# Performance work log

Hardware: AMD Instinct MI355X
Metric: run time of the kernel (lower is better)

Reference implementation:

```python
import jax, jax.numpy as jnp
import numpy as np

N = 40000      # nodes
E = 640000     # edges
G = 2048       # graphs
D = 128        # emb_dim
T = 10         # num_tasks
L = 5          # layers
ATOM_VOCAB = 64
BOND_VOCAB = 8
BN_EPS = 1e-5


def _bn(x, g, b, m, v):
    # inference-mode BatchNorm1d with running stats
    return (x - m) * jax.lax.rsqrt(v + BN_EPS) * g + b


def setup_inputs() -> dict:
    key = jax.random.key(0)
    ks = jax.random.split(key, 24)
    inp = {
        "x_atom": jax.random.randint(ks[0], (N, 9), 0, ATOM_VOCAB),
        "edge_index": jax.random.randint(ks[1], (2, E), 0, N),
        "edge_attr": jax.random.randint(ks[2], (E, 3), 0, BOND_VOCAB),
        "batch": jnp.sort(jax.random.randint(ks[3], (N,), 0, G)),
        # embedding tables
        "atom_emb": jax.random.normal(ks[4], (9, ATOM_VOCAB, D)) * 0.1,
        "bond_emb": jax.random.normal(ks[5], (L, 3, BOND_VOCAB, D)) * 0.1,
        # per-layer GIN params (stacked over L)
        "eps": jnp.zeros((L,)),
        "W1": jax.random.normal(ks[6], (L, D, 2 * D)) * 0.05,
        "b1": jnp.zeros((L, 2 * D)),
        "g1": jnp.ones((L, 2 * D)),
        "bt1": jnp.zeros((L, 2 * D)),
        "m1": jax.random.normal(ks[7], (L, 2 * D)) * 0.1,
        "v1": jax.random.uniform(ks[8], (L, 2 * D), minval=0.5, maxval=1.5),
        "W2": jax.random.normal(ks[9], (L, 2 * D, D)) * 0.05,
        "b2": jnp.zeros((L, D)),
        # outer BatchNorm per layer
        "gO": jnp.ones((L, D)),
        "btO": jnp.zeros((L, D)),
        "mO": jax.random.normal(ks[10], (L, D)) * 0.1,
        "vO": jax.random.uniform(ks[11], (L, D), minval=0.5, maxval=1.5),
        # prediction head
        "Wp": jax.random.normal(ks[12], (D, T)) * 0.05,
        "bp": jnp.zeros((T,)),
    }
    return inp


def reference(x_atom, edge_index, edge_attr, batch, atom_emb, bond_emb, eps,
              W1, b1, g1, bt1, m1, v1, W2, b2, gO, btO, mO, vO, Wp, bp):
    src, dst = edge_index[0], edge_index[1]
    # AtomEncoder: sum of per-feature embeddings -> [N, D]
    x = atom_emb[jnp.arange(9)[None, :], x_atom].sum(axis=1)
    feat3 = jnp.arange(3)[None, :]
    for i in range(L):
        # BondEncoder for this layer -> [E, D]
        e = bond_emb[i][feat3, edge_attr].sum(axis=1)
        # message: relu(x_j + edge_emb); aggregate: scatter-add at dst
        msg = jax.nn.relu(x[src] + e)
        agg = jax.ops.segment_sum(msg, dst, num_segments=N)
        h = (1.0 + eps[i]) * x + agg
        # MLP: Linear -> BN -> ReLU -> Linear
        h = jax.nn.relu(_bn(h @ W1[i] + b1[i], g1[i], bt1[i], m1[i], v1[i]))
        h = h @ W2[i] + b2[i]
        # outer BN; ReLU after all but last layer (dropout = identity in eval)
        x = _bn(h, gO[i], btO[i], mO[i], vO[i])
        if i < L - 1:
            x = jax.nn.relu(x)
    # global mean pool over graphs
    sums = jax.ops.segment_sum(x, batch, num_segments=G)
    cnt = jax.ops.segment_sum(jnp.ones((N,), x.dtype), batch, num_segments=G)
    pooled = sums / jnp.maximum(cnt, 1.0)[:, None]
    return pooled @ Wp + bp
```

## Files before the change

### kernel.cpp

```cpp
#include <hip/hip_runtime.h>
#include <hip/hip_bf16.h>

#define NN 40000
#define NE 640000
#define NG 2048
#define DD 128
#define NT 10
#define NL 5
#define NB 80

typedef __attribute__((ext_vector_type(8))) short short8;
typedef __attribute__((ext_vector_type(4))) float f32x4;
typedef unsigned short ushort_t;

static __device__ __forceinline__ ushort_t f2b(float f) {
    return __bfloat16_as_ushort(__float2bfloat16(f));
}
static __device__ __forceinline__ float b2f(ushort_t u) {
    return __bfloat162float(__ushort_as_bfloat16(u));
}

__global__ void __launch_bounds__(256)
k_setup(const float* __restrict__ W1, const float* __restrict__ W2,
        const float* __restrict__ bemb, const int* __restrict__ xa,
        const float* __restrict__ aemb, const int* __restrict__ ei,
        ushort_t* __restrict__ W1P, ushort_t* __restrict__ W2P,
        ushort_t* __restrict__ ebsum16, ushort_t* __restrict__ x16,
        int* __restrict__ deg) {
    int b = blockIdx.x, t = threadIdx.x;
    if (b < 1280) {
        int tid = b * 256 + t;
        int layer = tid >> 16;
        int r = tid & 65535;
        int half = r >> 15;
        int q = r & 32767;
        int j = q & 7;
        int lane = (q >> 3) & 63;
        if (half == 0) {
            int kk = (q >> 9) & 3;
            int nt = q >> 11;
            int n = nt * 16 + (lane & 15);
            int k = kk * 32 + (lane >> 4) * 8 + j;
            W1P[layer * 32768 + q] = f2b(W1[(layer * DD + k) * 256 + n]);
        } else {
            int kk = (q >> 9) & 7;
            int nt = q >> 12;
            int n = nt * 16 + (lane & 15);
            int k = kk * 32 + (lane >> 4) * 8 + j;
            W2P[layer * 32768 + q] = f2b(W2[(layer * 256 + k) * DD + n]);
        }
        int d = tid & 127;
        int c = (tid >> 7) & 511;
        const float* bl = bemb + (size_t)layer * 3 * 8 * DD;
        ebsum16[tid] = f2b(bl[(c & 7) * DD + d] + bl[(8 + ((c >> 3) & 7)) * DD + d] +
                           bl[(16 + (c >> 6)) * DD + d]);
    } else if (b < 21280) {
        int half = t >> 7, d = t & 127;
        int n = (b - 1280) * 2 + half;
        __shared__ int idx[2][9];
        if (d < 9) idx[half][d] = xa[n * 9 + d];
        __syncthreads();
        float s = 0.f;
#pragma unroll
        for (int f = 0; f < 9; ++f) s += aemb[(f * 64 + idx[half][f]) * DD + d];
        x16[n * DD + d] = f2b(s);
    } else {
        int e = (b - 21280) * 256 + t;
        atomicAdd(&deg[ei[NE + e]], 1);
    }
}


__global__ void k_scan1(const int* __restrict__ deg, int* __restrict__ off,
                        int* __restrict__ blksum) {
    int b = blockIdx.x, t = threadIdx.x;
    int i = b * 256 + t;
    __shared__ int s[256];
    int v = (i < NN) ? deg[i] : 0;
    s[t] = v;
    __syncthreads();
    for (int d = 1; d < 256; d <<= 1) {
        int add = (t >= d) ? s[t - d] : 0;
        __syncthreads();
        s[t] += add;
        __syncthreads();
    }
    if (i <= NN) off[i] = s[t] - v;
    if (t == 255) blksum[b] = s[255];
}

__global__ void k_scan2(int* __restrict__ blk) {
    int t = threadIdx.x;
    __shared__ int s[256];
    int v = blk[t];
    s[t] = v;
    __syncthreads();
    for (int d = 1; d < 256; d <<= 1) {
        int add = (t >= d) ? s[t - d] : 0;
        __syncthreads();
        s[t] += add;
        __syncthreads();
    }
    blk[256 + t] = s[t] - v;
}

__global__ void k_scan3(int* __restrict__ off, const int* __restrict__ blk) {
    int b = blockIdx.x, t = threadIdx.x;
    int i = b * 256 + t;
    if (i <= NN) off[i] += blk[256 + b];
}

__global__ void __launch_bounds__(256)
k_bucket(const int* __restrict__ ei, const int* __restrict__ ea,
         const int* __restrict__ off, int* __restrict__ gbk,
         int2* __restrict__ ebuf) {
    __shared__ int hist[NB];
    __shared__ int sbase[NB];
    int t = threadIdx.x;
    int e0 = blockIdx.x * 1024;
    if (t < NB) hist[t] = 0;
    __syncthreads();
    int rank[4], buck[4], rec[4], dstv[4];
#pragma unroll
    for (int k = 0; k < 4; ++k) {
        int e = e0 + k * 256 + t;
        int src = ei[e];
        int dst = ei[NE + e];
        int a0 = ea[e * 3 + 0], a1 = ea[e * 3 + 1], a2 = ea[e * 3 + 2];
        rec[k] = src | ((a0 | (a1 << 3) | (a2 << 6)) << 16);
        dstv[k] = dst;
        int b = dst >> 9;
        buck[k] = b;
        rank[k] = atomicAdd(&hist[b], 1);
    }
    __syncthreads();
    if (t < NB) sbase[t] = atomicAdd(&gbk[t], hist[t]);
    __syncthreads();
#pragma unroll
    for (int k = 0; k < 4; ++k) {
        int b = buck[k];
        int slot = off[b << 9] + sbase[b] + rank[k];
        ebuf[slot] = make_int2(rec[k], dstv[k]);
    }
}

__global__ void k_scatter2(const int2* __restrict__ ebuf, const int* __restrict__ off,
                           int* __restrict__ cursor, int2* __restrict__ epack) {
    int i = blockIdx.x * 256 + threadIdx.x;
    int2 s = ebuf[i];
    int dst = s.y;
    int p = off[dst] + atomicAdd(&cursor[dst], 1);
    epack[p] = make_int2(s.x & 0xFFFF, s.x >> 16);
}

__global__ void __launch_bounds__(256)
k_gather(const ushort_t* __restrict__ xin, const int* __restrict__ off,
         const int2* __restrict__ epack, const ushort_t* __restrict__ ebsum16,
         const float* __restrict__ eps, int layer, ushort_t* __restrict__ h16) {
    int t = threadIdx.x;
    int lane = t & 63;
    int n = blockIdx.x * 4 + (t >> 6);
    const ushort2* x2 = (const ushort2*)xin;
    const ushort2* eb2 = (const ushort2*)ebsum16;
    ushort2 xv = x2[n * 64 + lane];
    float es = 1.f + eps[layer];
    float ax = es * b2f(xv.x), ay = es * b2f(xv.y);
    int p = off[n], p1 = off[n + 1];

    int2 e[8], f[8];
    bool have = (p + 8 <= p1);
    if (have) {
#pragma unroll
        for (int k = 0; k < 8; ++k) e[k] = epack[p + k];
    }
    while (have) {
        int np = p + 8;
        bool nh = (np + 8 <= p1);
        if (nh) {
#pragma unroll
            for (int k = 0; k < 8; ++k) f[k] = epack[np + k];
        }
        ushort2 vv[8], ss[8];
#pragma unroll
        for (int k = 0; k < 8; ++k) {
            vv[k] = eb2[e[k].y * 64 + lane];
            ss[k] = x2[e[k].x * 64 + lane];
        }
#pragma unroll
        for (int k = 0; k < 8; ++k) {
            ax += fmaxf(b2f(vv[k].x) + b2f(ss[k].x), 0.f);
            ay += fmaxf(b2f(vv[k].y) + b2f(ss[k].y), 0.f);
        }
        p = np;
#pragma unroll
        for (int k = 0; k < 8; ++k) e[k] = f[k];
        have = nh;
    }
    if (p + 4 <= p1) {
        int2 e4[4];
#pragma unroll
        for (int k = 0; k < 4; ++k) e4[k] = epack[p + k];
        ushort2 vv[4], ss[4];
#pragma unroll
        for (int k = 0; k < 4; ++k) {
            vv[k] = eb2[e4[k].y * 64 + lane];
            ss[k] = x2[e4[k].x * 64 + lane];
        }
#pragma unroll
        for (int k = 0; k < 4; ++k) {
            ax += fmaxf(b2f(vv[k].x) + b2f(ss[k].x), 0.f);
            ay += fmaxf(b2f(vv[k].y) + b2f(ss[k].y), 0.f);
        }
        p += 4;
    }
    for (; p < p1; ++p) {
        int2 er = epack[p];
        ushort2 ev = eb2[er.y * 64 + lane];
        ushort2 sv = x2[er.x * 64 + lane];
        ax += fmaxf(b2f(ev.x) + b2f(sv.x), 0.f);
        ay += fmaxf(b2f(ev.y) + b2f(sv.y), 0.f);
    }
    ushort2 o;
    o.x = f2b(ax);
    o.y = f2b(ay);
    ((ushort2*)h16)[n * 64 + lane] = o;
}

__global__ void __launch_bounds__(256)
k_mlp_mfma(const ushort_t* __restrict__ h16, const ushort_t* __restrict__ W1P,
           const ushort_t* __restrict__ W2P, const float* __restrict__ b1,
           const float* __restrict__ g1, const float* __restrict__ bt1,
           const float* __restrict__ m1, const float* __restrict__ v1,
           const float* __restrict__ b2_, const float* __restrict__ gO,
           const float* __restrict__ btO, const float* __restrict__ mO,
           const float* __restrict__ vO, int relu, ushort_t* __restrict__ xout) {
    __shared__ ushort_t aS[32 * 136];
    __shared__ ushort_t mid[32 * 264];
    int t = threadIdx.x;
    int wave = t >> 6, lane = t & 63;
    int row0 = blockIdx.x * 32;
    int lrow = lane & 15, quad = lane >> 4;

#pragma unroll
    for (int ps = 0; ps < 2; ++ps) {
        int idx = ps * 256 + t;
        int r = idx >> 4, c = (idx & 15) * 8;
        *(short8*)&aS[r * 136 + c] = *(const short8*)&h16[(row0 + r) * DD + c];
    }
    __syncthreads();

    f32x4 acc1[2][4];
#pragma unroll
    for (int rt = 0; rt < 2; ++rt)
#pragma unroll
        for (int i = 0; i < 4; ++i) acc1[rt][i] = (f32x4){0.f, 0.f, 0.f, 0.f};
#pragma unroll
    for (int kk = 0; kk < 4; ++kk) {
        short8 af0 = *(const short8*)&aS[lrow * 136 + kk * 32 + quad * 8];
        short8 af1 = *(const short8*)&aS[(16 + lrow) * 136 + kk * 32 + quad * 8];
#pragma unroll
        for (int i = 0; i < 4; ++i) {
            int nt = wave * 4 + i;
            short8 bf = *(const short8*)&W1P[((nt * 4 + kk) * 64 + lane) * 8];
            acc1[0][i] = __builtin_amdgcn_mfma_f32_16x16x32_bf16(af0, bf, acc1[0][i], 0, 0, 0);
            acc1[1][i] = __builtin_amdgcn_mfma_f32_16x16x32_bf16(af1, bf, acc1[1][i], 0, 0, 0);
        }
    }
#pragma unroll
    for (int i = 0; i < 4; ++i) {
        int col = (wave * 4 + i) * 16 + lrow;
        float s1 = g1[col] * rsqrtf(v1[col] + 1e-5f);
        float sh = bt1[col] - (m1[col] - b1[col]) * s1;
#pragma unroll
        for (int rt = 0; rt < 2; ++rt)
#pragma unroll
            for (int r = 0; r < 4; ++r) {
                int row = rt * 16 + quad * 4 + r;
                float o = acc1[rt][i][r] * s1 + sh;
                mid[row * 264 + col] = f2b(fmaxf(o, 0.f));
            }
    }
    __syncthreads();

    f32x4 acc2[2][2];
#pragma unroll
    for (int rt = 0; rt < 2; ++rt)
#pragma unroll
        for (int i = 0; i < 2; ++i) acc2[rt][i] = (f32x4){0.f, 0.f, 0.f, 0.f};
#pragma unroll
    for (int kk = 0; kk < 8; ++kk) {
        short8 af0 = *(const short8*)&mid[lrow * 264 + kk * 32 + quad * 8];
        short8 af1 = *(const short8*)&mid[(16 + lrow) * 264 + kk * 32 + quad * 8];
#pragma unroll
        for (int i = 0; i < 2; ++i) {
            int nt = wave * 2 + i;
            short8 bf = *(const short8*)&W2P[((nt * 8 + kk) * 64 + lane) * 8];
            acc2[0][i] = __builtin_amdgcn_mfma_f32_16x16x32_bf16(af0, bf, acc2[0][i], 0, 0, 0);
            acc2[1][i] = __builtin_amdgcn_mfma_f32_16x16x32_bf16(af1, bf, acc2[1][i], 0, 0, 0);
        }
    }
#pragma unroll
    for (int i = 0; i < 2; ++i) {
        int col = (wave * 2 + i) * 16 + lrow;
        float s = gO[col] * rsqrtf(vO[col] + 1e-5f);
        float sh = btO[col] - (mO[col] - b2_[col]) * s;
#pragma unroll
        for (int rt = 0; rt < 2; ++rt)
#pragma unroll
            for (int r = 0; r < 4; ++r) {
                int row = rt * 16 + quad * 4 + r;
                float o = acc2[rt][i][r] * s + sh;
                if (relu) o = fmaxf(o, 0.f);
                xout[(row0 + row) * DD + col] = f2b(o);
            }
    }
}

__global__ void k_poolhead(const ushort_t* __restrict__ x16,
                           const int* __restrict__ batch,
                           const float* __restrict__ Wp, const float* __restrict__ bp,
                           float* __restrict__ out) {
    int g = blockIdx.x, d = threadIdx.x;
    int lo = 0, hi = NN;
    while (lo < hi) { int m = (lo + hi) >> 1; if (batch[m] < g) lo = m + 1; else hi = m; }
    int start = lo;
    hi = NN;
    while (lo < hi) { int m = (lo + hi) >> 1; if (batch[m] < g + 1) lo = m + 1; else hi = m; }
    int end = lo;
    float s = 0.f;
    for (int n = start; n < end; ++n) s += b2f(x16[n * DD + d]);
    float c = fmaxf((float)(end - start), 1.f);
    __shared__ float p[DD];
    p[d] = s / c;
    __syncthreads();
    if (d < NT) {
        float acc = bp[d];
#pragma unroll 8
        for (int k = 0; k < DD; ++k) acc = fmaf(p[k], Wp[k * NT + d], acc);
        out[g * NT + d] = acc;
    }
}

extern "C" void kernel_launch(void* const* d_in, const int* in_sizes, int n_in,
                              void* d_out, int out_size, void* d_ws, size_t ws_size,
                              hipStream_t stream) {
    const int* x_atom = (const int*)d_in[0];
    const int* edge_index = (const int*)d_in[1];
    const int* edge_attr = (const int*)d_in[2];
    const int* batch = (const int*)d_in[3];
    const float* atom_emb = (const float*)d_in[4];
    const float* bond_emb = (const float*)d_in[5];
    const float* eps = (const float*)d_in[6];
    const float* W1 = (const float*)d_in[7];
    const float* b1 = (const float*)d_in[8];
    const float* g1 = (const float*)d_in[9];
    const float* bt1 = (const float*)d_in[10];
    const float* m1 = (const float*)d_in[11];
    const float* v1 = (const float*)d_in[12];
    const float* W2 = (const float*)d_in[13];
    const float* b2 = (const float*)d_in[14];
    const float* gO = (const float*)d_in[15];
    const float* btO = (const float*)d_in[16];
    const float* mO = (const float*)d_in[17];
    const float* vO = (const float*)d_in[18];
    const float* Wp = (const float*)d_in[19];
    const float* bp = (const float*)d_in[20];

    ushort_t* x16a = (ushort_t*)d_ws;
    ushort_t* x16b = x16a + NN * DD;
    ushort_t* h16 = x16b + NN * DD;
    ushort_t* W1P = h16 + NN * DD;
    ushort_t* W2P = W1P + NL * 32768;
    ushort_t* ebsum16 = W2P + NL * 32768;
    int* deg = (int*)(ebsum16 + NL * 65536);
    int* off = deg + NN;
    int* blk = off + 40064;
    int* cursor = blk + 512;
    int* gbk = cursor + NN;
    int2* epack = (int2*)(gbk + 128);
    int2* ebuf = epack + NE;

    hipMemsetAsync(deg, 0, (NN + 40064 + 512 + NN + 128) * sizeof(int), stream);

    k_setup<<<23780, 256, 0, stream>>>(W1, W2, bond_emb, x_atom, atom_emb,
                                       edge_index, W1P, W2P, ebsum16, x16a, deg);
    k_scan1<<<157, 256, 0, stream>>>(deg, off, blk);
    k_scan2<<<1, 256, 0, stream>>>(blk);
    k_scan3<<<157, 256, 0, stream>>>(off, blk);
    k_bucket<<<NE / 1024, 256, 0, stream>>>(edge_index, edge_attr, off, gbk, ebuf);
    k_scatter2<<<NE / 256, 256, 0, stream>>>(ebuf, off, cursor, epack);

    for (int i = 0; i < NL; ++i) {
        ushort_t* xin = (i & 1) ? x16b : x16a;
        ushort_t* xout = (i & 1) ? x16a : x16b;
        k_gather<<<NN / 4, 256, 0, stream>>>(xin, off, epack, ebsum16 + i * 65536,
                                             eps, i, h16);
        k_mlp_mfma<<<NN / 32, 256, 0, stream>>>(
            h16, W1P + (size_t)i * 32768, W2P + (size_t)i * 32768, b1 + i * 256,
            g1 + i * 256, bt1 + i * 256, m1 + i * 256, v1 + i * 256, b2 + i * DD,
            gO + i * DD, btO + i * DD, mO + i * DD, vO + i * DD,
            (i < NL - 1) ? 1 : 0, xout);
    }
    k_poolhead<<<NG, DD, 0, stream>>>(x16b, batch, Wp, bp, (float*)d_out);
}
```

Measured before the change: 411.7 us.

## Gather edge messages with 16-byte loads, four edges per wave in parallel

```diff
diff --git a/kernel.cpp b/kernel.cpp
--- a/kernel.cpp
+++ b/kernel.cpp
@@ -153,77 +153,78 @@
     epack[p] = make_int2(s.x & 0xFFFF, s.x >> 16);
 }
 
-__global__ void __launch_bounds__(256)
+__global__ void __launch_bounds__(256, 8)
 k_gather(const ushort_t* __restrict__ xin, const int* __restrict__ off,
          const int2* __restrict__ epack, const ushort_t* __restrict__ ebsum16,
          const float* __restrict__ eps, int layer, ushort_t* __restrict__ h16) {
     int t = threadIdx.x;
     int lane = t & 63;
     int n = blockIdx.x * 4 + (t >> 6);
-    const ushort2* x2 = (const ushort2*)xin;
-    const ushort2* eb2 = (const ushort2*)ebsum16;
-    ushort2 xv = x2[n * 64 + lane];
-    float es = 1.f + eps[layer];
-    float ax = es * b2f(xv.x), ay = es * b2f(xv.y);
-    int p = off[n], p1 = off[n + 1];
-
-    int2 e[8], f[8];
-    bool have = (p + 8 <= p1);
-    if (have) {
-#pragma unroll
-        for (int k = 0; k < 8; ++k) e[k] = epack[p + k];
-    }
-    while (have) {
-        int np = p + 8;
-        bool nh = (np + 8 <= p1);
-        if (nh) {
-#pragma unroll
-            for (int k = 0; k < 8; ++k) f[k] = epack[np + k];
+    int g = lane >> 4;
+    int dcol = lane & 15;
+    const short8* x8 = (const short8*)xin;
+    const short8* eb8 = (const short8*)ebsum16;
+    int p0 = off[n], p1 = off[n + 1];
+
+    float acc[8];
+#pragma unroll
+    for (int k = 0; k < 8; ++k) acc[k] = 0.f;
+
+    short8 sR0{}, vR0{}, sR1{}, vR1{};
+    bool mR0 = false, mR1 = false;
+    int2 eI{};
+    bool mI = false;
+
+    if (p0 < p1) {
+        bool m = (p0 + g < p1);
+        int2 e = epack[m ? (p0 + g) : p0];
+        if (m) { sR0 = x8[(size_t)e.x * 16 + dcol]; vR0 = eb8[e.y * 16 + dcol]; }
+        mR0 = m;
+    }
+    if (p0 + 4 < p1) {
+        bool m = (p0 + 4 + g < p1);
+        int2 e = epack[m ? (p0 + 4 + g) : (p0 + 4)];
+        if (m) { sR1 = x8[(size_t)e.x * 16 + dcol]; vR1 = eb8[e.y * 16 + dcol]; }
+        mR1 = m;
+    }
+    if (p0 + 8 < p1) {
+        mI = (p0 + 8 + g < p1);
+        eI = epack[mI ? (p0 + 8 + g) : (p0 + 8)];
+    }
+
+    for (int p = p0; p < p1; p += 4) {
+        short8 sR2{}, vR2{};
+        bool mR2 = mI;
+        if (mR2) { sR2 = x8[(size_t)eI.x * 16 + dcol]; vR2 = eb8[eI.y * 16 + dcol]; }
+        mI = false;
+        if (p + 12 < p1) {
+            mI = (p + 12 + g < p1);
+            eI = epack[mI ? (p + 12 + g) : (p + 12)];
         }
-        ushort2 vv[8], ss[8];
-#pragma unroll
-        for (int k = 0; k < 8; ++k) {
-            vv[k] = eb2[e[k].y * 64 + lane];
-            ss[k] = x2[e[k].x * 64 + lane];
+        if (mR0) {
+#pragma unroll
+            for (int k = 0; k < 8; ++k)
+                acc[k] += fmaxf(b2f((ushort_t)sR0[k]) + b2f((ushort_t)vR0[k]), 0.f);
         }
-#pragma unroll
-        for (int k = 0; k < 8; ++k) {
-            ax += fmaxf(b2f(vv[k].x) + b2f(ss[k].x), 0.f);
-            ay += fmaxf(b2f(vv[k].y) + b2f(ss[k].y), 0.f);
-        }
-        p = np;
-#pragma unroll
-        for (int k = 0; k < 8; ++k) e[k] = f[k];
-        have = nh;
-    }
-    if (p + 4 <= p1) {
-        int2 e4[4];
-#pragma unroll
-        for (int k = 0; k < 4; ++k) e4[k] = epack[p + k];
-        ushort2 vv[4], ss[4];
-#pragma unroll
-        for (int k = 0; k < 4; ++k) {
-            vv[k] = eb2[e4[k].y * 64 + lane];
-            ss[k] = x2[e4[k].x * 64 + lane];
-        }
-#pragma unroll
-        for (int k = 0; k < 4; ++k) {
-            ax += fmaxf(b2f(vv[k].x) + b2f(ss[k].x), 0.f);
-            ay += fmaxf(b2f(vv[k].y) + b2f(ss[k].y), 0.f);
-        }
-        p += 4;
-    }
-    for (; p < p1; ++p) {
-        int2 er = epack[p];
-        ushort2 ev = eb2[er.y * 64 + lane];
-        ushort2 sv = x2[er.x * 64 + lane];
-        ax += fmaxf(b2f(ev.x) + b2f(sv.x), 0.f);
-        ay += fmaxf(b2f(ev.y) + b2f(sv.y), 0.f);
-    }
-    ushort2 o;
-    o.x = f2b(ax);
-    o.y = f2b(ay);
-    ((ushort2*)h16)[n * 64 + lane] = o;
+        sR0 = sR1; vR0 = vR1; mR0 = mR1;
+        sR1 = sR2; vR1 = vR2; mR1 = mR2;
+    }
+
+#pragma unroll
+    for (int k = 0; k < 8; ++k) {
+        acc[k] += __shfl_xor(acc[k], 16, 64);
+        acc[k] += __shfl_xor(acc[k], 32, 64);
+    }
+
+    if (g == 0) {
+        float es = 1.f + eps[layer];
+        short8 xv = x8[(size_t)n * 16 + dcol];
+        short8 o;
+#pragma unroll
+        for (int k = 0; k < 8; ++k)
+            o[k] = (short)f2b(acc[k] + es * b2f((ushort_t)xv[k]));
+        *(short8*)&h16[(size_t)n * DD + dcol * 8] = o;
+    }
 }
 
 __global__ void __launch_bounds__(256)
```

Result: slower. 420.3 us (+2.1%).

## Pack edge records into one int and double MLP row tile to 64

Applied to the files above, without the earlier changes.

```diff
diff --git a/kernel.cpp b/kernel.cpp
--- a/kernel.cpp
+++ b/kernel.cpp
@@ -145,17 +145,17 @@
 }
 
 __global__ void k_scatter2(const int2* __restrict__ ebuf, const int* __restrict__ off,
-                           int* __restrict__ cursor, int2* __restrict__ epack) {
+                           int* __restrict__ cursor, int* __restrict__ epack) {
     int i = blockIdx.x * 256 + threadIdx.x;
     int2 s = ebuf[i];
     int dst = s.y;
     int p = off[dst] + atomicAdd(&cursor[dst], 1);
-    epack[p] = make_int2(s.x & 0xFFFF, s.x >> 16);
-}
-
-__global__ void __launch_bounds__(256)
+    epack[p] = s.x;
+}
+
+__global__ void __launch_bounds__(256, 8)
 k_gather(const ushort_t* __restrict__ xin, const int* __restrict__ off,
-         const int2* __restrict__ epack, const ushort_t* __restrict__ ebsum16,
+         const int* __restrict__ epack, const ushort_t* __restrict__ ebsum16,
          const float* __restrict__ eps, int layer, ushort_t* __restrict__ h16) {
     int t = threadIdx.x;
     int lane = t & 63;
@@ -167,7 +167,7 @@
     float ax = es * b2f(xv.x), ay = es * b2f(xv.y);
     int p = off[n], p1 = off[n + 1];
 
-    int2 e[8], f[8];
+    int e[8], f[8];
     bool have = (p + 8 <= p1);
     if (have) {
 #pragma unroll
@@ -183,8 +183,8 @@
         ushort2 vv[8], ss[8];
 #pragma unroll
         for (int k = 0; k < 8; ++k) {
-            vv[k] = eb2[e[k].y * 64 + lane];
-            ss[k] = x2[e[k].x * 64 + lane];
+            vv[k] = eb2[(e[k] >> 16) * 64 + lane];
+            ss[k] = x2[(e[k] & 0xFFFF) * 64 + lane];
         }
 #pragma unroll
         for (int k = 0; k < 8; ++k) {
@@ -197,14 +197,14 @@
         have = nh;
     }
     if (p + 4 <= p1) {
-        int2 e4[4];
+        int e4[4];
 #pragma unroll
         for (int k = 0; k < 4; ++k) e4[k] = epack[p + k];
         ushort2 vv[4], ss[4];
 #pragma unroll
         for (int k = 0; k < 4; ++k) {
-            vv[k] = eb2[e4[k].y * 64 + lane];
-            ss[k] = x2[e4[k].x * 64 + lane];
+            vv[k] = eb2[(e4[k] >> 16) * 64 + lane];
+            ss[k] = x2[(e4[k] & 0xFFFF) * 64 + lane];
         }
 #pragma unroll
         for (int k = 0; k < 4; ++k) {
@@ -214,9 +214,9 @@
         p += 4;
     }
     for (; p < p1; ++p) {
-        int2 er = epack[p];
-        ushort2 ev = eb2[er.y * 64 + lane];
-        ushort2 sv = x2[er.x * 64 + lane];
+        int er = epack[p];
+        ushort2 ev = eb2[(er >> 16) * 64 + lane];
+        ushort2 sv = x2[(er & 0xFFFF) * 64 + lane];
         ax += fmaxf(b2f(ev.x) + b2f(sv.x), 0.f);
         ay += fmaxf(b2f(ev.y) + b2f(sv.y), 0.f);
     }
@@ -234,36 +234,39 @@
            const float* __restrict__ b2_, const float* __restrict__ gO,
            const float* __restrict__ btO, const float* __restrict__ mO,
            const float* __restrict__ vO, int relu, ushort_t* __restrict__ xout) {
-    __shared__ ushort_t aS[32 * 136];
-    __shared__ ushort_t mid[32 * 264];
+    __shared__ ushort_t aS[64 * 136];
+    __shared__ ushort_t mid[64 * 264];
     int t = threadIdx.x;
     int wave = t >> 6, lane = t & 63;
-    int row0 = blockIdx.x * 32;
+    int row0 = blockIdx.x * 64;
     int lrow = lane & 15, quad = lane >> 4;
 
 #pragma unroll
-    for (int ps = 0; ps < 2; ++ps) {
+    for (int ps = 0; ps < 4; ++ps) {
         int idx = ps * 256 + t;
         int r = idx >> 4, c = (idx & 15) * 8;
         *(short8*)&aS[r * 136 + c] = *(const short8*)&h16[(row0 + r) * DD + c];
     }
     __syncthreads();
 
-    f32x4 acc1[2][4];
-#pragma unroll
-    for (int rt = 0; rt < 2; ++rt)
+    f32x4 acc1[4][4];
+#pragma unroll
+    for (int rt = 0; rt < 4; ++rt)
 #pragma unroll
         for (int i = 0; i < 4; ++i) acc1[rt][i] = (f32x4){0.f, 0.f, 0.f, 0.f};
 #pragma unroll
     for (int kk = 0; kk < 4; ++kk) {
-        short8 af0 = *(const short8*)&aS[lrow * 136 + kk * 32 + quad * 8];
-        short8 af1 = *(const short8*)&aS[(16 + lrow) * 136 + kk * 32 + quad * 8];
+        short8 af[4];
+#pragma unroll
+        for (int rt = 0; rt < 4; ++rt)
+            af[rt] = *(const short8*)&aS[(rt * 16 + lrow) * 136 + kk * 32 + quad * 8];
 #pragma unroll
         for (int i = 0; i < 4; ++i) {
             int nt = wave * 4 + i;
             short8 bf = *(const short8*)&W1P[((nt * 4 + kk) * 64 + lane) * 8];
-            acc1[0][i] = __builtin_amdgcn_mfma_f32_16x16x32_bf16(af0, bf, acc1[0][i], 0, 0, 0);
-            acc1[1][i] = __builtin_amdgcn_mfma_f32_16x16x32_bf16(af1, bf, acc1[1][i], 0, 0, 0);
+#pragma unroll
+            for (int rt = 0; rt < 4; ++rt)
+                acc1[rt][i] = __builtin_amdgcn_mfma_f32_16x16x32_bf16(af[rt], bf, acc1[rt][i], 0, 0, 0);
         }
     }
 #pragma unroll
@@ -272,7 +275,7 @@
         float s1 = g1[col] * rsqrtf(v1[col] + 1e-5f);
         float sh = bt1[col] - (m1[col] - b1[col]) * s1;
 #pragma unroll
-        for (int rt = 0; rt < 2; ++rt)
+        for (int rt = 0; rt < 4; ++rt)
 #pragma unroll
             for (int r = 0; r < 4; ++r) {
                 int row = rt * 16 + quad * 4 + r;
@@ -282,21 +285,24 @@
     }
     __syncthreads();
 
-    f32x4 acc2[2][2];
-#pragma unroll
-    for (int rt = 0; rt < 2; ++rt)
+    f32x4 acc2[4][2];
+#pragma unroll
+    for (int rt = 0; rt < 4; ++rt)
 #pragma unroll
         for (int i = 0; i < 2; ++i) acc2[rt][i] = (f32x4){0.f, 0.f, 0.f, 0.f};
 #pragma unroll
     for (int kk = 0; kk < 8; ++kk) {
-        short8 af0 = *(const short8*)&mid[lrow * 264 + kk * 32 + quad * 8];
-        short8 af1 = *(const short8*)&mid[(16 + lrow) * 264 + kk * 32 + quad * 8];
+        short8 af[4];
+#pragma unroll
+        for (int rt = 0; rt < 4; ++rt)
+            af[rt] = *(const short8*)&mid[(rt * 16 + lrow) * 264 + kk * 32 + quad * 8];
 #pragma unroll
         for (int i = 0; i < 2; ++i) {
             int nt = wave * 2 + i;
             short8 bf = *(const short8*)&W2P[((nt * 8 + kk) * 64 + lane) * 8];
-            acc2[0][i] = __builtin_amdgcn_mfma_f32_16x16x32_bf16(af0, bf, acc2[0][i], 0, 0, 0);
-            acc2[1][i] = __builtin_amdgcn_mfma_f32_16x16x32_bf16(af1, bf, acc2[1][i], 0, 0, 0);
+#pragma unroll
+            for (int rt = 0; rt < 4; ++rt)
+                acc2[rt][i] = __builtin_amdgcn_mfma_f32_16x16x32_bf16(af[rt], bf, acc2[rt][i], 0, 0, 0);
         }
     }
 #pragma unroll
@@ -305,7 +311,7 @@
         float s = gO[col] * rsqrtf(vO[col] + 1e-5f);
         float sh = btO[col] - (mO[col] - b2_[col]) * s;
 #pragma unroll
-        for (int rt = 0; rt < 2; ++rt)
+        for (int rt = 0; rt < 4; ++rt)
 #pragma unroll
             for (int r = 0; r < 4; ++r) {
                 int row = rt * 16 + quad * 4 + r;
@@ -377,8 +383,8 @@
     int* blk = off + 40064;
     int* cursor = blk + 512;
     int* gbk = cursor + NN;
-    int2* epack = (int2*)(gbk + 128);
-    int2* ebuf = epack + NE;
+    int* epack = gbk + 128;
+    int2* ebuf = (int2*)(epack + NE);
 
     hipMemsetAsync(deg, 0, (NN + 40064 + 512 + NN + 128) * sizeof(int), stream);
 
@@ -395,7 +401,7 @@
         ushort_t* xout = (i & 1) ? x16a : x16b;
         k_gather<<<NN / 4, 256, 0, stream>>>(xin, off, epack, ebsum16 + i * 65536,
                                              eps, i, h16);
-        k_mlp_mfma<<<NN / 32, 256, 0, stream>>>(
+        k_mlp_mfma<<<NN / 64, 256, 0, stream>>>(
             h16, W1P + (size_t)i * 32768, W2P + (size_t)i * 32768, b1 + i * 256,
             g1 + i * 256, bt1 + i * 256, m1 + i * 256, v1 + i * 256, b2 + i * DD,
             gO + i * DD, btO + i * DD, mO + i * DD, vO + i * DD,
```

Result: slower. 421.4 us (+2.4%).

## Gather neighbor features from an fp8 copy and pack edge records into one int

Applied to the files above, without the earlier changes.

```diff
diff --git a/kernel.cpp b/kernel.cpp
--- a/kernel.cpp
+++ b/kernel.cpp
@@ -12,12 +12,16 @@
 typedef __attribute__((ext_vector_type(8))) short short8;
 typedef __attribute__((ext_vector_type(4))) float f32x4;
 typedef unsigned short ushort_t;
+typedef unsigned char uchar_t;
 
 static __device__ __forceinline__ ushort_t f2b(float f) {
     return __bfloat16_as_ushort(__float2bfloat16(f));
 }
 static __device__ __forceinline__ float b2f(ushort_t u) {
     return __bfloat162float(__ushort_as_bfloat16(u));
+}
+static __device__ __forceinline__ uchar_t f2p8(float f) {
+    return (uchar_t)(__builtin_amdgcn_cvt_pk_fp8_f32(f, 0.f, 0, false) & 0xFF);
 }
 
 __global__ void __launch_bounds__(256)
@@ -26,7 +30,7 @@
         const float* __restrict__ aemb, const int* __restrict__ ei,
         ushort_t* __restrict__ W1P, ushort_t* __restrict__ W2P,
         ushort_t* __restrict__ ebsum16, ushort_t* __restrict__ x16,
-        int* __restrict__ deg) {
+        uchar_t* __restrict__ x8, int* __restrict__ deg) {
     int b = blockIdx.x, t = threadIdx.x;
     if (b < 1280) {
         int tid = b * 256 + t;
@@ -64,6 +68,7 @@
 #pragma unroll
         for (int f = 0; f < 9; ++f) s += aemb[(f * 64 + idx[half][f]) * DD + d];
         x16[n * DD + d] = f2b(s);
+        x8[n * DD + d] = f2p8(s);
     } else {
         int e = (b - 21280) * 256 + t;
         atomicAdd(&deg[ei[NE + e]], 1);
@@ -145,29 +150,31 @@
 }
 
 __global__ void k_scatter2(const int2* __restrict__ ebuf, const int* __restrict__ off,
-                           int* __restrict__ cursor, int2* __restrict__ epack) {
+                           int* __restrict__ cursor, int* __restrict__ epack) {
     int i = blockIdx.x * 256 + threadIdx.x;
     int2 s = ebuf[i];
     int dst = s.y;
     int p = off[dst] + atomicAdd(&cursor[dst], 1);
-    epack[p] = make_int2(s.x & 0xFFFF, s.x >> 16);
+    epack[p] = s.x;
 }
 
 __global__ void __launch_bounds__(256)
-k_gather(const ushort_t* __restrict__ xin, const int* __restrict__ off,
-         const int2* __restrict__ epack, const ushort_t* __restrict__ ebsum16,
-         const float* __restrict__ eps, int layer, ushort_t* __restrict__ h16) {
+k_gather(const ushort_t* __restrict__ xin, const uchar_t* __restrict__ x8in,
+         const int* __restrict__ off, const int* __restrict__ epack,
+         const ushort_t* __restrict__ ebsum16, const float* __restrict__ eps,
+         int layer, ushort_t* __restrict__ h16) {
     int t = threadIdx.x;
     int lane = t & 63;
     int n = blockIdx.x * 4 + (t >> 6);
     const ushort2* x2 = (const ushort2*)xin;
+    const ushort_t* x8r = (const ushort_t*)x8in;
     const ushort2* eb2 = (const ushort2*)ebsum16;
     ushort2 xv = x2[n * 64 + lane];
     float es = 1.f + eps[layer];
     float ax = es * b2f(xv.x), ay = es * b2f(xv.y);
     int p = off[n], p1 = off[n + 1];
 
-    int2 e[8], f[8];
+    int e[8], f[8];
     bool have = (p + 8 <= p1);
     if (have) {
 #pragma unroll
@@ -180,16 +187,19 @@
 #pragma unroll
             for (int k = 0; k < 8; ++k) f[k] = epack[np + k];
         }
-        ushort2 vv[8], ss[8];
+        ushort2 vv[8];
+        ushort_t sp[8];
 #pragma unroll
         for (int k = 0; k < 8; ++k) {
-            vv[k] = eb2[e[k].y * 64 + lane];
-            ss[k] = x2[e[k].x * 64 + lane];
+            vv[k] = eb2[(e[k] >> 16) * 64 + lane];
+            sp[k] = x8r[(e[k] & 0xFFFF) * 64 + lane];
         }
 #pragma unroll
         for (int k = 0; k < 8; ++k) {
-            ax += fmaxf(b2f(vv[k].x) + b2f(ss[k].x), 0.f);
-            ay += fmaxf(b2f(vv[k].y) + b2f(ss[k].y), 0.f);
+            float sx = __builtin_amdgcn_cvt_f32_fp8((int)sp[k], 0);
+            float sy = __builtin_amdgcn_cvt_f32_fp8((int)sp[k], 1);
+            ax += fmaxf(b2f(vv[k].x) + sx, 0.f);
+            ay += fmaxf(b2f(vv[k].y) + sy, 0.f);
         }
         p = np;
 #pragma unroll
@@ -197,28 +207,31 @@
         have = nh;
     }
     if (p + 4 <= p1) {
-        int2 e4[4];
+        int e4[4];
 #pragma unroll
         for (int k = 0; k < 4; ++k) e4[k] = epack[p + k];
-        ushort2 vv[4], ss[4];
+        ushort2 vv[4];
+        ushort_t sp[4];
 #pragma unroll
         for (int k = 0; k < 4; ++k) {
-            vv[k] = eb2[e4[k].y * 64 + lane];
-            ss[k] = x2[e4[k].x * 64 + lane];
+            vv[k] = eb2[(e4[k] >> 16) * 64 + lane];
+            sp[k] = x8r[(e4[k] & 0xFFFF) * 64 + lane];
         }
 #pragma unroll
         for (int k = 0; k < 4; ++k) {
-            ax += fmaxf(b2f(vv[k].x) + b2f(ss[k].x), 0.f);
-            ay += fmaxf(b2f(vv[k].y) + b2f(ss[k].y), 0.f);
+            float sx = __builtin_amdgcn_cvt_f32_fp8((int)sp[k], 0);
+            float sy = __builtin_amdgcn_cvt_f32_fp8((int)sp[k], 1);
+            ax += fmaxf(b2f(vv[k].x) + sx, 0.f);
+            ay += fmaxf(b2f(vv[k].y) + sy, 0.f);
         }
         p += 4;
     }
     for (; p < p1; ++p) {
-        int2 er = epack[p];
-        ushort2 ev = eb2[er.y * 64 + lane];
-        ushort2 sv = x2[er.x * 64 + lane];
-        ax += fmaxf(b2f(ev.x) + b2f(sv.x), 0.f);
-        ay += fmaxf(b2f(ev.y) + b2f(sv.y), 0.f);
+        int er = epack[p];
+        ushort2 ev = eb2[(er >> 16) * 64 + lane];
+        ushort_t sv = x8r[(er & 0xFFFF) * 64 + lane];
+        ax += fmaxf(b2f(ev.x) + __builtin_amdgcn_cvt_f32_fp8((int)sv, 0), 0.f);
+        ay += fmaxf(b2f(ev.y) + __builtin_amdgcn_cvt_f32_fp8((int)sv, 1), 0.f);
     }
     ushort2 o;
     o.x = f2b(ax);
@@ -233,7 +246,8 @@
            const float* __restrict__ m1, const float* __restrict__ v1,
            const float* __restrict__ b2_, const float* __restrict__ gO,
            const float* __restrict__ btO, const float* __restrict__ mO,
-           const float* __restrict__ vO, int relu, ushort_t* __restrict__ xout) {
+           const float* __restrict__ vO, int relu, ushort_t* __restrict__ xout,
+           uchar_t* __restrict__ x8out) {
     __shared__ ushort_t aS[32 * 136];
     __shared__ ushort_t mid[32 * 264];
     int t = threadIdx.x;
@@ -266,6 +280,7 @@
             acc1[1][i] = __builtin_amdgcn_mfma_f32_16x16x32_bf16(af1, bf, acc1[1][i], 0, 0, 0);
         }
     }
+    __syncthreads();
 #pragma unroll
     for (int i = 0; i < 4; ++i) {
         int col = (wave * 4 + i) * 16 + lrow;
@@ -299,6 +314,7 @@
             acc2[1][i] = __builtin_amdgcn_mfma_f32_16x16x32_bf16(af1, bf, acc2[1][i], 0, 0, 0);
         }
     }
+    uchar_t* s8 = (uchar_t*)aS;
 #pragma unroll
     for (int i = 0; i < 2; ++i) {
         int col = (wave * 2 + i) * 16 + lrow;
@@ -312,8 +328,11 @@
                 float o = acc2[rt][i][r] * s + sh;
                 if (relu) o = fmaxf(o, 0.f);
                 xout[(row0 + row) * DD + col] = f2b(o);
+                s8[row * DD + col] = f2p8(o);
             }
     }
+    __syncthreads();
+    ((int4*)(x8out + (size_t)row0 * DD))[t] = ((const int4*)s8)[t];
 }
 
 __global__ void k_poolhead(const ushort_t* __restrict__ x16,
@@ -372,18 +391,20 @@
     ushort_t* W1P = h16 + NN * DD;
     ushort_t* W2P = W1P + NL * 32768;
     ushort_t* ebsum16 = W2P + NL * 32768;
-    int* deg = (int*)(ebsum16 + NL * 65536);
+    uchar_t* x8a = (uchar_t*)(ebsum16 + NL * 65536);
+    uchar_t* x8b = x8a + NN * DD;
+    int* deg = (int*)(x8b + NN * DD);
     int* off = deg + NN;
     int* blk = off + 40064;
     int* cursor = blk + 512;
     int* gbk = cursor + NN;
-    int2* epack = (int2*)(gbk + 128);
-    int2* ebuf = epack + NE;
+    int* epack = gbk + 128;
+    int2* ebuf = (int2*)(epack + NE);
 
     hipMemsetAsync(deg, 0, (NN + 40064 + 512 + NN + 128) * sizeof(int), stream);
 
     k_setup<<<23780, 256, 0, stream>>>(W1, W2, bond_emb, x_atom, atom_emb,
-                                       edge_index, W1P, W2P, ebsum16, x16a, deg);
+                                       edge_index, W1P, W2P, ebsum16, x16a, x8a, deg);
     k_scan1<<<157, 256, 0, stream>>>(deg, off, blk);
     k_scan2<<<1, 256, 0, stream>>>(blk);
     k_scan3<<<157, 256, 0, stream>>>(off, blk);
@@ -393,13 +414,15 @@
     for (int i = 0; i < NL; ++i) {
         ushort_t* xin = (i & 1) ? x16b : x16a;
         ushort_t* xout = (i & 1) ? x16a : x16b;
-        k_gather<<<NN / 4, 256, 0, stream>>>(xin, off, epack, ebsum16 + i * 65536,
-                                             eps, i, h16);
+        uchar_t* x8in = (i & 1) ? x8b : x8a;
+        uchar_t* x8out = (i & 1) ? x8a : x8b;
+        k_gather<<<NN / 4, 256, 0, stream>>>(xin, x8in, off, epack,
+                                             ebsum16 + i * 65536, eps, i, h16);
         k_mlp_mfma<<<NN / 32, 256, 0, stream>>>(
             h16, W1P + (size_t)i * 32768, W2P + (size_t)i * 32768, b1 + i * 256,
             g1 + i * 256, bt1 + i * 256, m1 + i * 256, v1 + i * 256, b2 + i * DD,
             gO + i * DD, btO + i * DD, mO + i * DD, vO + i * DD,
-            (i < NL - 1) ? 1 : 0, xout);
+            (i < NL - 1) ? 1 : 0, xout, x8out);
     }
     k_poolhead<<<NG, DD, 0, stream>>>(x16b, batch, Wp, bp, (float*)d_out);
 }
```

New measurement: 410.2 us. No clear change (-0.4%).
